# Kernel tuning notes

Measured on AMD Instinct MI355X. Metric: run time of the kernel, lower is better.

Reference implementation:

```python
import jax, jax.numpy as jnp
import numpy as np

D = 2048; H = 16; KV = 4; HD = D // H  # head_dim=128
EPS = 1e-6; THETA = 10000.0


def _rmsnorm(x, w):
    # x: [..., HD]
    var = jnp.mean(x * x, axis=-1, keepdims=True)
    return x * jax.lax.rsqrt(var + EPS) * w


def _rope(x, cos, sin):
    # x: [B, L, nH, HD]; cos/sin: [L, HD//2]; interleaved-pair rotation
    xe = x[..., 0::2]
    xo = x[..., 1::2]
    c = cos[None, :, None, :]
    s = sin[None, :, None, :]
    re = xe * c - xo * s
    ro = xe * s + xo * c
    return jnp.stack([re, ro], axis=-1).reshape(x.shape)


def setup_inputs() -> dict:
    key = jax.random.key(0)
    ks = jax.random.split(key, 8)
    B, L = 2, 2048
    x = jax.random.normal(ks[0], (B, L, D), dtype=jnp.float32)
    wq = jax.random.normal(ks[1], (D, D), dtype=jnp.float32) * 0.02
    wk = jax.random.normal(ks[2], (KV * HD, D), dtype=jnp.float32) * 0.02
    wv = jax.random.normal(ks[3], (KV * HD, D), dtype=jnp.float32) * 0.02
    wo = jax.random.normal(ks[4], (D, D), dtype=jnp.float32) * 0.02
    q_norm_w = jnp.ones((HD,), dtype=jnp.float32)
    k_norm_w = jnp.ones((HD,), dtype=jnp.float32)
    return {"x": x, "wq": wq, "wk": wk, "wv": wv, "wo": wo,
            "q_norm_w": q_norm_w, "k_norm_w": k_norm_w}


def reference(x, wq, wk, wv, wo, q_norm_w, k_norm_w):
    B, L, _ = x.shape
    G = H // KV  # GQA group size (repeat factor)

    q = (x @ wq.T).reshape(B, L, H, HD)
    k = (x @ wk.T).reshape(B, L, KV, HD)
    v = (x @ wv.T).reshape(B, L, KV, HD)

    q = _rmsnorm(q, q_norm_w)
    k = _rmsnorm(k, k_norm_w)

    # RoPE (positions 0..L-1, prompt path)
    inv_freq = 1.0 / (THETA ** (jnp.arange(0, HD, 2, dtype=jnp.float32) / HD))
    ang = jnp.arange(L, dtype=jnp.float32)[:, None] * inv_freq[None, :]  # [L, HD/2]
    cos, sin = jnp.cos(ang), jnp.sin(ang)
    q = _rope(q, cos, sin)
    k = _rope(k, cos, sin)

    # GQA: q head h attends kv head h // G (== repeat_interleave of k,v)
    qg = q.reshape(B, L, KV, G, HD)
    scale = 1.0 / jnp.sqrt(jnp.float32(HD))
    scores = jnp.einsum('bqkgd,bskd->bkgqs', qg, k) * scale  # [B,KV,G,L,L]

    causal = jnp.tril(jnp.ones((L, L), dtype=bool))
    scores = jnp.where(causal, scores, jnp.finfo(scores.dtype).min)
    p = jax.nn.softmax(scores, axis=-1)

    o = jnp.einsum('bkgqs,bskd->bqkgd', p, v).reshape(B, L, D)
    return o @ wo.T
```

## Files before the change

### kernel.cpp

```cpp
#include <hip/hip_runtime.h>
#include <hip/hip_bf16.h>
#include <stdint.h>
#include <stddef.h>

#define D_DIM 2048
#define H_HEADS 16
#define KV_HEADS 4
#define HEAD_DIM 128
#define SEQ_L 2048
#define BATCH 2
#define NTOK 4096
#define NQK 2560
#define NQKV 3072

typedef __attribute__((ext_vector_type(4))) float f32x4;
typedef __attribute__((ext_vector_type(16))) float f32x16;
typedef __attribute__((ext_vector_type(8))) short bf16x8;

__device__ __forceinline__ unsigned short f2bf(float f) {
  __hip_bfloat16 h = __float2bfloat16(f);
  return *reinterpret_cast<unsigned short*>(&h);
}
__device__ __forceinline__ unsigned pack2(float lo, float hi) {
  return (unsigned)f2bf(lo) | ((unsigned)f2bf(hi) << 16);
}
__device__ __forceinline__ float bf2f(unsigned short s) {
  return __uint_as_float(((unsigned int)s) << 16);
}

__device__ __forceinline__ void async_copy16(const void* g, void* l) {
  __builtin_amdgcn_global_load_lds(
      (__attribute__((address_space(1))) void*)(g),
      (__attribute__((address_space(3))) void*)(l),
      16, 0, 0);
}

__device__ __forceinline__ void cast_seg(const float* __restrict__ src,
                                         unsigned short* __restrict__ dst,
                                         int n4, int gid, int stride) {
  for (int i = gid; i < n4; i += stride) {
    float4 v = *reinterpret_cast<const float4*>(src + i * 4);
    uint2 o;
    o.x = pack2(v.x, v.y);
    o.y = pack2(v.z, v.w);
    *reinterpret_cast<uint2*>(dst + i * 4) = o;
  }
}

__global__ __launch_bounds__(256) void fused_cast_kernel(
    const float* __restrict__ s0, const float* __restrict__ s1,
    const float* __restrict__ s2, const float* __restrict__ s3,
    const float* __restrict__ s4,
    unsigned short* __restrict__ d0, unsigned short* __restrict__ d1,
    unsigned short* __restrict__ d2, unsigned short* __restrict__ d3,
    unsigned short* __restrict__ d4) {
  int gid = blockIdx.x * blockDim.x + threadIdx.x;
  int stride = gridDim.x * blockDim.x;
  cast_seg(s0, d0, (NTOK * D_DIM) / 4, gid, stride);
  cast_seg(s1, d1, (D_DIM * D_DIM) / 4, gid, stride);
  cast_seg(s2, d2, (512 * D_DIM) / 4, gid, stride);
  cast_seg(s3, d3, (512 * D_DIM) / 4, gid, stride);
  cast_seg(s4, d4, (D_DIM * D_DIM) / 4, gid, stride);
}

__global__ __launch_bounds__(256) void rope_table_kernel(float* __restrict__ cosT,
                                                         float* __restrict__ sinT) {
  int i = blockIdx.x * blockDim.x + threadIdx.x;
  if (i >= SEQ_L * 64) return;
  int p = i & 63;
  float l = (float)(i >> 6);
  float inv = powf(10000.0f, -(float)p / 64.0f);
  float ang = l * inv;
  cosT[i] = cosf(ang);
  sinT[i] = sinf(ang);
}

__device__ __forceinline__ void store_out(unsigned short* p, float v) { *p = f2bf(v); }
__device__ __forceinline__ void store_out(float* p, float v) { *p = v; }

template <typename OutT, bool VSPLIT>
__global__ __launch_bounds__(256) void gemm_bt_kernel(const unsigned short* __restrict__ A,
                                                      const unsigned short* __restrict__ B,
                                                      OutT* __restrict__ C,
                                                      unsigned short* __restrict__ vt,
                                                      int M, int N, int K) {
  __shared__ unsigned short Alds[128 * 32];
  __shared__ unsigned short Blds[128 * 32];
  const int tid = threadIdx.x;
  const int wave = tid >> 6;
  const int lane = tid & 63;
  const int l15 = lane & 15;
  const int l4 = lane >> 4;

  const int nwg = gridDim.x * gridDim.y;
  const int orig = blockIdx.y * gridDim.x + blockIdx.x;
  const int cpx = nwg >> 3;
  const int swz = (orig & 7) * cpx + (orig >> 3);
  const int m0 = (swz % gridDim.x) * 128;
  const int n0 = (swz / gridDim.x) * 128;

  const int wm = (wave >> 1) * 64;
  const int wn = (wave & 1) * 64;

  f32x4 acc[4][4] = {};

  const int soff0 = wave * 1024 + lane * 16;

  for (int kt = 0; kt < K; kt += 32) {
#pragma unroll
    for (int inst = 0; inst < 2; ++inst) {
      int off = soff0 + inst * 4096;
      int row = off >> 6;
      int colb = off & 63;
      const char* ga = (const char*)(A + (size_t)(m0 + row) * K + kt) + colb;
      async_copy16(ga, (char*)Alds + off);
      const char* gb = (const char*)(B + (size_t)(n0 + row) * K + kt) + colb;
      async_copy16(gb, (char*)Blds + off);
    }
    __syncthreads();
    bf16x8 af[4], bfr[4];
#pragma unroll
    for (int i = 0; i < 4; ++i)
      af[i] = *reinterpret_cast<const bf16x8*>(Alds + (wm + i * 16 + l15) * 32 + l4 * 8);
#pragma unroll
    for (int j = 0; j < 4; ++j)
      bfr[j] = *reinterpret_cast<const bf16x8*>(Blds + (wn + j * 16 + l15) * 32 + l4 * 8);
#pragma unroll
    for (int i = 0; i < 4; ++i)
#pragma unroll
      for (int j = 0; j < 4; ++j)
        acc[i][j] = __builtin_amdgcn_mfma_f32_16x16x32_bf16(af[i], bfr[j], acc[i][j], 0, 0, 0);
    __syncthreads();
  }

  if (VSPLIT && n0 >= NQK) {
#pragma unroll
    for (int i = 0; i < 4; ++i)
#pragma unroll
      for (int j = 0; j < 4; ++j) {
        int vrow = n0 + wn + j * 16 + l15 - NQK;
        int tok0 = m0 + wm + i * 16 + l4 * 4;
        ushort4 pk;
        pk.x = f2bf(acc[i][j][0]);
        pk.y = f2bf(acc[i][j][1]);
        pk.z = f2bf(acc[i][j][2]);
        pk.w = f2bf(acc[i][j][3]);
        *reinterpret_cast<ushort4*>(vt + (size_t)vrow * NTOK + tok0) = pk;
      }
    return;
  }

  const int cstride = VSPLIT ? NQK : N;
#pragma unroll
  for (int i = 0; i < 4; ++i)
#pragma unroll
    for (int j = 0; j < 4; ++j) {
      int col = n0 + wn + j * 16 + l15;
#pragma unroll
      for (int r = 0; r < 4; ++r) {
        int row = m0 + wm + i * 16 + l4 * 4 + r;
        store_out(C + (size_t)row * cstride + col, acc[i][j][r]);
      }
    }
}

__global__ __launch_bounds__(256) void norm_rope_kernel(unsigned short* __restrict__ qk,
                                                        const float* __restrict__ qw,
                                                        const float* __restrict__ kw,
                                                        const float* __restrict__ cosT,
                                                        const float* __restrict__ sinT) {
  int wid = (blockIdx.x * blockDim.x + threadIdx.x) >> 6;
  int lane = threadIdx.x & 63;
  unsigned short* rowp;
  const float* w;
  int m;
  float sc;
  if (wid < NTOK * H_HEADS) {
    m = wid >> 4;
    int hh = wid & 15;
    rowp = qk + (size_t)m * NQK + hh * HEAD_DIM;
    w = qw;
    sc = 0.08838834764831845f;
  } else {
    int r2 = wid - NTOK * H_HEADS;
    m = r2 >> 2;
    int kvh = r2 & 3;
    rowp = qk + (size_t)m * NQK + D_DIM + kvh * HEAD_DIM;
    w = kw;
    sc = 1.0f;
  }
  int l = m & (SEQ_L - 1);
  unsigned int pair = *reinterpret_cast<const unsigned int*>(rowp + lane * 2);
  float e = bf2f((unsigned short)(pair & 0xffffu));
  float o = bf2f((unsigned short)(pair >> 16));
  float ss = e * e + o * o;
#pragma unroll
  for (int off = 1; off < 64; off <<= 1) ss += __shfl_xor(ss, off);
  float rsn = rsqrtf(ss * (1.0f / 128.0f) + 1e-6f) * sc;
  float we = w[lane * 2], wo_ = w[lane * 2 + 1];
  float c = cosT[l * 64 + lane], s = sinT[l * 64 + lane];
  float xe = e * rsn * we, xo = o * rsn * wo_;
  float re = xe * c - xo * s;
  float ro = xe * s + xo * c;
  *reinterpret_cast<unsigned int*>(rowp + lane * 2) = pack2(re, ro);
}

__global__ __launch_bounds__(256, 2) void attn_kernel(const unsigned short* __restrict__ qk,
                                                      const unsigned short* __restrict__ vt,
                                                      unsigned short* __restrict__ obuf,
                                                      unsigned short* __restrict__ p2,
                                                      float* __restrict__ m1G, float* __restrict__ l1G,
                                                      float* __restrict__ m2G, float* __restrict__ l2G) {
  __shared__ unsigned short Kl[2][64 * 128];
  __shared__ unsigned short Vl[2][128 * 64];
  __shared__ float invl[128];

  const int tid = threadIdx.x;
  const int w = tid >> 6, lane = tid & 63;
  const int l31 = lane & 31, hi = lane >> 5;

  const int jx = blockIdx.x;
  int qt, seg, kv_begin, kv_end;
  bool split;
  if (jx < 16) {
    split = true;
    qt = 15 - (jx >> 1);
    seg = jx & 1;
    int nt = qt + 1;
    kv_begin = seg * nt;
    kv_end = kv_begin + nt;
  } else {
    split = false;
    seg = 0;
    qt = 23 - jx;
    kv_begin = 0;
    kv_end = 2 * qt + 2;
  }
  const int q0 = qt * 128;

  const int bh = blockIdx.y;
  const int b = bh >> 4, h = bh & 15, kvh = h >> 2;

  const unsigned short* Qg = qk + (size_t)(b * SEQ_L + q0 + w * 32 + l31) * NQK + h * HEAD_DIM;
  const unsigned short* Kg = qk + (size_t)(b * SEQ_L) * NQK + D_DIM + kvh * HEAD_DIM;
  const unsigned short* Vg = vt + (size_t)(kvh * HEAD_DIM) * NTOK + b * SEQ_L;

  bf16x8 qf[8];
#pragma unroll
  for (int kk = 0; kk < 8; ++kk)
    qf[kk] = *reinterpret_cast<const bf16x8*>(Qg + kk * 16 + hi * 8);

  f32x16 accO[4] = {};
  float m_run = -1e30f, l_run = 0.0f;

  const int qmin_w = q0 + w * 32;
  const int qmax_w = qmin_w + 31;
  const int qg = qmin_w + l31;

  auto stage = [&](int bb, int kt) {
#pragma unroll
    for (int i = 0; i < 4; ++i) {
      int o = (i * 256 + tid) * 16;
      {
        int row = o >> 8;
        int scb = (o & 255) ^ ((row & 7) << 4);
        const char* src = (const char*)(Kg + (size_t)(kt * 64 + row) * NQK) + scb;
        async_copy16(src, (char*)(&Kl[bb][0]) + o);
      }
      {
        int d = o >> 7;
        int skb = (o & 127) ^ ((d & 7) << 4);
        const char* src = (const char*)(Vg + (size_t)d * NTOK + kt * 64) + skb;
        async_copy16(src, (char*)(&Vl[bb][0]) + o);
      }
    }
  };

  stage(0, kv_begin);
  asm volatile("s_waitcnt vmcnt(0)" ::: "memory");
  __syncthreads();

  int buf = 0;
  for (int kt = kv_begin; kt < kv_end; ++kt) {
    if (kt + 1 < kv_end) stage(buf ^ 1, kt + 1);

    if (kt * 64 <= qmax_w) {
      f32x16 st[2] = {};
      __builtin_amdgcn_s_setprio(1);
#pragma unroll
      for (int stile = 0; stile < 2; ++stile) {
#pragma unroll
        for (int kk = 0; kk < 8; ++kk) {
          int row = stile * 32 + l31;
          int off = (row << 8) + (((kk << 5) + (hi << 4)) ^ ((l31 & 7) << 4));
          bf16x8 kf = *reinterpret_cast<const bf16x8*>((const char*)(&Kl[buf][0]) + off);
          st[stile] = __builtin_amdgcn_mfma_f32_32x32x16_bf16(kf, qf[kk], st[stile], 0, 0, 0);
        }
      }
      __builtin_amdgcn_s_setprio(0);

      const bool need_mask = (kt * 64 + 63 > qmin_w);
      float tmax = -1e30f;
#pragma unroll
      for (int stile = 0; stile < 2; ++stile)
#pragma unroll
        for (int r = 0; r < 16; ++r) {
          float s = st[stile][r];
          if (need_mask) {
            int key = kt * 64 + stile * 32 + (r & 3) + ((r >> 2) << 3) + (hi << 2);
            if (key > qg) s = -1e30f;
          }
          st[stile][r] = s;
          tmax = fmaxf(tmax, s);
        }
      tmax = fmaxf(tmax, __shfl_xor(tmax, 32));

      if (!__all(tmax - m_run <= 8.0f)) {
        float mnew = fmaxf(m_run, tmax);
        float corr = __expf(m_run - mnew);
        m_run = mnew;
        l_run *= corr;
        float corrq[16];
#pragma unroll
        for (int r = 0; r < 16; ++r) {
          int qi = (r & 3) + ((r >> 2) << 3) + (hi << 2);
          corrq[r] = __shfl(corr, qi);
        }
#pragma unroll
        for (int dt = 0; dt < 4; ++dt)
#pragma unroll
          for (int r = 0; r < 16; ++r) accO[dt][r] *= corrq[r];
      }

      float rsum = 0.0f;
#pragma unroll
      for (int stile = 0; stile < 2; ++stile)
#pragma unroll
        for (int r = 0; r < 16; ++r) {
          float pe = __expf(st[stile][r] - m_run);
          st[stile][r] = pe;
          rsum += pe;
        }
      rsum += __shfl_xor(rsum, 32);
      l_run += rsum;

      bf16x8 pa[2][2];
#pragma unroll
      for (int stile = 0; stile < 2; ++stile)
#pragma unroll
        for (int kc = 0; kc < 2; ++kc) {
          int rb = kc * 8;
          unsigned x0 = pack2(st[stile][rb + 0], st[stile][rb + 1]);
          unsigned y0 = pack2(st[stile][rb + 4], st[stile][rb + 5]);
          unsigned x1 = pack2(st[stile][rb + 2], st[stile][rb + 3]);
          unsigned y1 = pack2(st[stile][rb + 6], st[stile][rb + 7]);
          unsigned x0s = (unsigned)__shfl_xor((int)x0, 32);
          unsigned y0s = (unsigned)__shfl_xor((int)y0, 32);
          unsigned x1s = (unsigned)__shfl_xor((int)x1, 32);
          unsigned y1s = (unsigned)__shfl_xor((int)y1, 32);
          unsigned w0 = hi ? y0s : x0;
          unsigned w2 = hi ? y0 : x0s;
          unsigned w1 = hi ? y1s : x1;
          unsigned w3 = hi ? y1 : x1s;
          union { bf16x8 v; unsigned u[4]; } uu;
          uu.u[0] = w0; uu.u[1] = w1; uu.u[2] = w2; uu.u[3] = w3;
          pa[stile][kc] = uu.v;
        }

      __builtin_amdgcn_s_setprio(1);
#pragma unroll
      for (int dt = 0; dt < 4; ++dt) {
        int drow = dt * 32 + l31;
#pragma unroll
        for (int stile = 0; stile < 2; ++stile)
#pragma unroll
          for (int kc = 0; kc < 2; ++kc) {
            int off = (drow << 7) + (((stile << 6) + (kc << 5) + (hi << 4)) ^ ((l31 & 7) << 4));
            bf16x8 vf = *reinterpret_cast<const bf16x8*>((const char*)(&Vl[buf][0]) + off);
            accO[dt] = __builtin_amdgcn_mfma_f32_32x32x16_bf16(pa[stile][kc], vf, accO[dt], 0, 0, 0);
          }
      }
      __builtin_amdgcn_s_setprio(0);
    }

    asm volatile("s_waitcnt vmcnt(0)" ::: "memory");
    __syncthreads();
    buf ^= 1;
  }

  if (!split) {
    if (hi == 0) invl[w * 32 + l31] = 1.0f / l_run;
    __syncthreads();
#pragma unroll
    for (int dt = 0; dt < 4; ++dt)
#pragma unroll
      for (int r = 0; r < 16; ++r) {
        int qrow = (r & 3) + ((r >> 2) << 3) + (hi << 2);
        float val = accO[dt][r] * invl[w * 32 + qrow];
        int tok = b * SEQ_L + q0 + w * 32 + qrow;
        obuf[(size_t)tok * D_DIM + h * HEAD_DIM + dt * 32 + l31] = f2bf(val);
      }
  } else {
    const int rowbase = bh * 1024 + (qt - 8) * 128;
    if (hi == 0) {
      int rr = rowbase + w * 32 + l31;
      if (seg == 0) { m1G[rr] = m_run; l1G[rr] = l_run; }
      else          { m2G[rr] = m_run; l2G[rr] = l_run; }
    }
#pragma unroll
    for (int dt = 0; dt < 4; ++dt)
#pragma unroll
      for (int r = 0; r < 16; ++r) {
        int qrow = (r & 3) + ((r >> 2) << 3) + (hi << 2);
        float val = accO[dt][r];
        if (seg == 0) {
          int tok = b * SEQ_L + q0 + w * 32 + qrow;
          obuf[(size_t)tok * D_DIM + h * HEAD_DIM + dt * 32 + l31] = f2bf(val);
        } else {
          size_t prow = (size_t)(rowbase + w * 32 + qrow);
          p2[prow * HEAD_DIM + dt * 32 + l31] = f2bf(val);
        }
      }
  }
}

__global__ __launch_bounds__(256) void combine_kernel(unsigned short* __restrict__ obuf,
                                                      const unsigned short* __restrict__ p2,
                                                      const float* __restrict__ m1G, const float* __restrict__ l1G,
                                                      const float* __restrict__ m2G, const float* __restrict__ l2G) {
  int gid = blockIdx.x * blockDim.x + threadIdx.x;
  int row = gid >> 4;
  int dc = (gid & 15) * 8;
  int bh = row >> 10;
  int rem = row & 1023;
  int qt = 8 + (rem >> 7);
  int rr = rem & 127;
  int b = bh >> 4, h = bh & 15;
  size_t tok = (size_t)(b * SEQ_L + qt * 128 + rr);

  float m1 = m1G[row], l1 = l1G[row], m2 = m2G[row], l2 = l2G[row];
  float mm = fmaxf(m1, m2);
  float w1 = __expf(m1 - mm), w2 = __expf(m2 - mm);
  float inv = 1.0f / (w1 * l1 + w2 * l2);

  unsigned short* op = obuf + tok * D_DIM + h * HEAD_DIM + dc;
  const unsigned short* pp = p2 + (size_t)row * HEAD_DIM + dc;
  ushort4 a0 = *reinterpret_cast<const ushort4*>(op);
  ushort4 a1 = *reinterpret_cast<const ushort4*>(op + 4);
  ushort4 b0 = *reinterpret_cast<const ushort4*>(pp);
  ushort4 b1 = *reinterpret_cast<const ushort4*>(pp + 4);
  ushort4 o0, o1;
  o0.x = f2bf((w1 * bf2f(a0.x) + w2 * bf2f(b0.x)) * inv);
  o0.y = f2bf((w1 * bf2f(a0.y) + w2 * bf2f(b0.y)) * inv);
  o0.z = f2bf((w1 * bf2f(a0.z) + w2 * bf2f(b0.z)) * inv);
  o0.w = f2bf((w1 * bf2f(a0.w) + w2 * bf2f(b0.w)) * inv);
  o1.x = f2bf((w1 * bf2f(a1.x) + w2 * bf2f(b1.x)) * inv);
  o1.y = f2bf((w1 * bf2f(a1.y) + w2 * bf2f(b1.y)) * inv);
  o1.z = f2bf((w1 * bf2f(a1.z) + w2 * bf2f(b1.z)) * inv);
  o1.w = f2bf((w1 * bf2f(a1.w) + w2 * bf2f(b1.w)) * inv);
  *reinterpret_cast<ushort4*>(op) = o0;
  *reinterpret_cast<ushort4*>(op + 4) = o1;
}

extern "C" void kernel_launch(void* const* d_in, const int* in_sizes, int n_in,
                              void* d_out, int out_size, void* d_ws, size_t ws_size,
                              hipStream_t stream) {
  const float* x   = (const float*)d_in[0];
  const float* wq  = (const float*)d_in[1];
  const float* wk  = (const float*)d_in[2];
  const float* wv  = (const float*)d_in[3];
  const float* wo  = (const float*)d_in[4];
  const float* qnw = (const float*)d_in[5];
  const float* knw = (const float*)d_in[6];
  float* out = (float*)d_out;

  char* ws = (char*)d_ws;
  unsigned short* Xb    = (unsigned short*)(ws);
  unsigned short* Wqkvb = (unsigned short*)(ws + 16777216);
  unsigned short* Wob   = (unsigned short*)(ws + 29360128);
  unsigned short* QKb   = (unsigned short*)(ws + 37748736);
  unsigned short* VTb   = (unsigned short*)(ws + 58720256);
  unsigned short* Obuf  = (unsigned short*)(ws + 62914560);
  float* cosT = (float*)(ws + 79691776);
  float* sinT = (float*)(ws + 80216064);

  unsigned short* P2 = (unsigned short*)(ws);
  float* m1G = (float*)(ws + 8388608);
  float* l1G = (float*)(ws + 8519680);
  float* m2G = (float*)(ws + 8650752);
  float* l2G = (float*)(ws + 8781824);

  fused_cast_kernel<<<1024, 256, 0, stream>>>(
      x, wq, wk, wv, wo,
      Xb, Wqkvb,
      Wqkvb + (size_t)D_DIM * D_DIM,
      Wqkvb + (size_t)NQK * D_DIM,
      Wob);
  rope_table_kernel<<<512, 256, 0, stream>>>(cosT, sinT);

  dim3 g1(NTOK / 128, NQKV / 128);
  gemm_bt_kernel<unsigned short, true><<<g1, 256, 0, stream>>>(
      Xb, Wqkvb, QKb, VTb, NTOK, NQKV, D_DIM);

  norm_rope_kernel<<<(NTOK * (H_HEADS + KV_HEADS)) / 4, 256, 0, stream>>>(QKb, qnw, knw, cosT, sinT);

  attn_kernel<<<dim3(24, BATCH * H_HEADS), 256, 0, stream>>>(
      QKb, VTb, Obuf, P2, m1G, l1G, m2G, l2G);
  combine_kernel<<<2048, 256, 0, stream>>>(Obuf, P2, m1G, l1G, m2G, l2G);

  dim3 g2(NTOK / 128, D_DIM / 128);
  gemm_bt_kernel<float, false><<<g2, 256, 0, stream>>>(Obuf, Wob, out, nullptr, NTOK, D_DIM, D_DIM);
}
```

Before: 261.6 us.

## Single-buffer V via register staging, raise occupancy, use permlane32 swap

V tiles are now prefetched into registers and written to a single shared-memory buffer each iteration, while K stays double-buffered through async LDS copies. Halving V's LDS footprint lets launch bounds go from 2 to 3 blocks per CU for more latency hiding. The P-fragment exchange between wave halves uses v_permlane32_swap in place of four shuffles and selects. In exchange the loop gains an extra barrier, the V prefetch registers add pressure under the tighter register budget, and the synchronous V global loads may stall.

```diff
diff --git a/kernel.cpp b/kernel.cpp
--- a/kernel.cpp
+++ b/kernel.cpp
@@ -26,6 +26,9 @@
 }
 __device__ __forceinline__ float bf2f(unsigned short s) {
   return __uint_as_float(((unsigned int)s) << 16);
+}
+__device__ __forceinline__ void plane32swap(unsigned& a, unsigned& b) {
+  asm volatile("v_permlane32_swap_b32 %0, %1" : "+v"(a), "+v"(b));
 }
 
 __device__ __forceinline__ void async_copy16(const void* g, void* l) {
@@ -205,14 +208,14 @@
   *reinterpret_cast<unsigned int*>(rowp + lane * 2) = pack2(re, ro);
 }
 
-__global__ __launch_bounds__(256, 2) void attn_kernel(const unsigned short* __restrict__ qk,
+__global__ __launch_bounds__(256, 3) void attn_kernel(const unsigned short* __restrict__ qk,
                                                       const unsigned short* __restrict__ vt,
                                                       unsigned short* __restrict__ obuf,
                                                       unsigned short* __restrict__ p2,
                                                       float* __restrict__ m1G, float* __restrict__ l1G,
                                                       float* __restrict__ m2G, float* __restrict__ l2G) {
   __shared__ unsigned short Kl[2][64 * 128];
-  __shared__ unsigned short Vl[2][128 * 64];
+  __shared__ unsigned short Vl[128 * 64];
   __shared__ float invl[128];
 
   const int tid = threadIdx.x;
@@ -257,34 +260,54 @@
   const int qmax_w = qmin_w + 31;
   const int qg = qmin_w + l31;
 
-  auto stage = [&](int bb, int kt) {
+  auto stageK = [&](int bb, int kt) {
 #pragma unroll
     for (int i = 0; i < 4; ++i) {
       int o = (i * 256 + tid) * 16;
-      {
-        int row = o >> 8;
-        int scb = (o & 255) ^ ((row & 7) << 4);
-        const char* src = (const char*)(Kg + (size_t)(kt * 64 + row) * NQK) + scb;
-        async_copy16(src, (char*)(&Kl[bb][0]) + o);
-      }
-      {
-        int d = o >> 7;
-        int skb = (o & 127) ^ ((d & 7) << 4);
-        const char* src = (const char*)(Vg + (size_t)d * NTOK + kt * 64) + skb;
-        async_copy16(src, (char*)(&Vl[bb][0]) + o);
-      }
+      int row = o >> 8;
+      int scb = (o & 255) ^ ((row & 7) << 4);
+      const char* src = (const char*)(Kg + (size_t)(kt * 64 + row) * NQK) + scb;
+      async_copy16(src, (char*)(&Kl[bb][0]) + o);
     }
   };
-
-  stage(0, kv_begin);
-  asm volatile("s_waitcnt vmcnt(0)" ::: "memory");
-  __syncthreads();
+  auto loadV = [&](bf16x8* vr, int kt) {
+#pragma unroll
+    for (int i = 0; i < 4; ++i) {
+      int o = (i * 256 + tid) * 16;
+      int d = o >> 7;
+      const char* src = (const char*)(Vg + (size_t)d * NTOK + kt * 64) + (o & 127);
+      vr[i] = *reinterpret_cast<const bf16x8*>(src);
+    }
+  };
+  auto writeV = [&](const bf16x8* vr) {
+#pragma unroll
+    for (int i = 0; i < 4; ++i) {
+      int o = (i * 256 + tid) * 16;
+      int d = o >> 7;
+      int so = o ^ ((d & 7) << 4);
+      *reinterpret_cast<bf16x8*>((char*)Vl + so) = vr[i];
+    }
+  };
+
+  bf16x8 vrA[4], vrB[4];
+  stageK(0, kv_begin);
+  loadV(vrA, kv_begin);
 
   int buf = 0;
   for (int kt = kv_begin; kt < kv_end; ++kt) {
-    if (kt + 1 < kv_end) stage(buf ^ 1, kt + 1);
-
-    if (kt * 64 <= qmax_w) {
+    asm volatile("s_waitcnt vmcnt(0)" ::: "memory");
+    __syncthreads();
+
+    const bool par = ((kt - kv_begin) & 1) != 0;
+    if (!par) writeV(vrA); else writeV(vrB);
+    if (kt + 1 < kv_end) {
+      stageK(buf ^ 1, kt + 1);
+      if (!par) loadV(vrB, kt + 1); else loadV(vrA, kt + 1);
+    }
+
+    const bool active = (kt * 64 <= qmax_w);
+    bf16x8 pa[2][2];
+    if (active) {
       f32x16 st[2] = {};
       __builtin_amdgcn_s_setprio(1);
 #pragma unroll
@@ -344,29 +367,26 @@
       rsum += __shfl_xor(rsum, 32);
       l_run += rsum;
 
-      bf16x8 pa[2][2];
 #pragma unroll
       for (int stile = 0; stile < 2; ++stile)
 #pragma unroll
         for (int kc = 0; kc < 2; ++kc) {
           int rb = kc * 8;
-          unsigned x0 = pack2(st[stile][rb + 0], st[stile][rb + 1]);
-          unsigned y0 = pack2(st[stile][rb + 4], st[stile][rb + 5]);
-          unsigned x1 = pack2(st[stile][rb + 2], st[stile][rb + 3]);
-          unsigned y1 = pack2(st[stile][rb + 6], st[stile][rb + 7]);
-          unsigned x0s = (unsigned)__shfl_xor((int)x0, 32);
-          unsigned y0s = (unsigned)__shfl_xor((int)y0, 32);
-          unsigned x1s = (unsigned)__shfl_xor((int)x1, 32);
-          unsigned y1s = (unsigned)__shfl_xor((int)y1, 32);
-          unsigned w0 = hi ? y0s : x0;
-          unsigned w2 = hi ? y0 : x0s;
-          unsigned w1 = hi ? y1s : x1;
-          unsigned w3 = hi ? y1 : x1s;
+          unsigned a  = pack2(st[stile][rb + 0], st[stile][rb + 1]);
+          unsigned bw = pack2(st[stile][rb + 4], st[stile][rb + 5]);
+          unsigned c  = pack2(st[stile][rb + 2], st[stile][rb + 3]);
+          unsigned d  = pack2(st[stile][rb + 6], st[stile][rb + 7]);
+          plane32swap(a, bw);
+          plane32swap(c, d);
           union { bf16x8 v; unsigned u[4]; } uu;
-          uu.u[0] = w0; uu.u[1] = w1; uu.u[2] = w2; uu.u[3] = w3;
+          uu.u[0] = a; uu.u[1] = c; uu.u[2] = bw; uu.u[3] = d;
           pa[stile][kc] = uu.v;
         }
-
+    }
+
+    __syncthreads();
+
+    if (active) {
       __builtin_amdgcn_s_setprio(1);
 #pragma unroll
       for (int dt = 0; dt < 4; ++dt) {
@@ -376,15 +396,13 @@
 #pragma unroll
           for (int kc = 0; kc < 2; ++kc) {
             int off = (drow << 7) + (((stile << 6) + (kc << 5) + (hi << 4)) ^ ((l31 & 7) << 4));
-            bf16x8 vf = *reinterpret_cast<const bf16x8*>((const char*)(&Vl[buf][0]) + off);
+            bf16x8 vf = *reinterpret_cast<const bf16x8*>((const char*)Vl + off);
             accO[dt] = __builtin_amdgcn_mfma_f32_32x32x16_bf16(pa[stile][kc], vf, accO[dt], 0, 0, 0);
           }
       }
       __builtin_amdgcn_s_setprio(0);
     }
 
-    asm volatile("s_waitcnt vmcnt(0)" ::: "memory");
-    __syncthreads();
     buf ^= 1;
   }
 
```

Measured after the change: 346.8 us. 32.6% more time.
